# Performance work log

Measured on AMD Instinct MI355X. Metric: run time of the kernel, lower is better.

Reference implementation:

```python
import jax, jax.numpy as jnp
import numpy as np

B, L, D, W = 4, 256, 256, 8  # batch, seq_len, d_model, context_window
NS_EPS = 1e-7


def setup_inputs() -> dict:
    key = jax.random.key(0)
    ks = jax.random.split(key, 12)
    f = lambda k, s: jax.random.normal(k, s, dtype=jnp.float32)
    sD = 1.0 / np.sqrt(D)
    return {
        "x": f(ks[0], (B, L, D)),
        "k_aligned": jnp.tanh(f(ks[1], (B, L, D))),  # QKProjectionLayer applies tanh upstream
        "v": f(ks[2], (B, L, D)),
        "M_prev": f(ks[3], (B, D, D)) * 0.01,
        "S_prev": jnp.zeros((B, D, D), jnp.float32),
        # polynomial feature coeffs: phi(k) = c1*k + c2*k^2 (degree 2, dim-preserving)
        "poly_coeffs": jnp.stack([jnp.ones((D,), jnp.float32), 0.1 * jnp.ones((D,), jnp.float32)])
        + 0.01 * f(ks[4], (2, D)),
        "alpha_W": f(ks[5], (D, D)) * sD, "alpha_b": jnp.zeros((D,), jnp.float32),
        "eta_W": f(ks[6], (D, D)) * sD, "eta_b": jnp.zeros((D,), jnp.float32),
        "theta_W": f(ks[7], (D, D)) * sD, "theta_b": jnp.zeros((D,), jnp.float32),
        "gamma_W": f(ks[8], (D,)) * sD, "gamma_b": jnp.zeros((1,), jnp.float32),
        "out_W": f(ks[9], (D, D)) * sD, "out_b": jnp.zeros((D,), jnp.float32),
    }


def _newton_schulz_1(S):
    # NS_K with K=1: X <- 1.5*X - 0.5*X X^T X after Frobenius normalization
    norm = jnp.sqrt(jnp.sum(S * S, axis=(-2, -1), keepdims=True)) + NS_EPS
    X = S / norm
    return 1.5 * X - 0.5 * jnp.einsum('bij,bkj,bkl->bil', X, X, X)


def reference(x, k_aligned, v, M_prev, S_prev, poly_coeffs,
              alpha_W, alpha_b, eta_W, eta_b, theta_W, theta_b,
              gamma_W, gamma_b, out_W, out_b):
    Bn, Ln, Dn = x.shape
    # polynomial feature layer (dim-preserving, degree 2)
    k_phi = poly_coeffs[0] * k_aligned + poly_coeffs[1] * k_aligned ** 2  # [B,L,D]
    # per-token gates (precomputed, pure linear+sigmoid)
    alpha = jax.nn.sigmoid(x @ alpha_W.T + alpha_b)          # [B,L,D]
    eta = jax.nn.sigmoid(x @ eta_W.T + eta_b) * 0.1          # [B,L,D]
    theta = jax.nn.sigmoid(x @ theta_W.T + theta_b)          # [B,L,D]
    gamma = jax.nn.sigmoid(jnp.einsum('bld,d->bl', x, gamma_W) + gamma_b[0])  # [B,L]
    c_arr = jnp.minimum(jnp.arange(Ln) + 1, W).astype(x.dtype)  # actual window length per step

    to_t = lambda a: jnp.moveaxis(a, 1, 0)  # [B,L,...] -> [L,B,...]
    xs = (to_t(k_phi), to_t(v), to_t(gamma), to_t(alpha), to_t(eta), to_t(theta), c_arr)

    buf_k = jnp.zeros((Bn, W, Dn), x.dtype)  # sliding window of phi(k); zero pads contribute 0
    buf_v = jnp.zeros((Bn, W, Dn), x.dtype)
    buf_g = jnp.zeros((Bn, W), x.dtype)

    def step(carry, xt):
        M, S, bk, bv, bg = carry
        k_t, v_t, g_t, a_t, e_t, th_t, c_t = xt
        bk = jnp.concatenate([bk[:, 1:], k_t[:, None]], axis=1)
        bv = jnp.concatenate([bv[:, 1:], v_t[:, None]], axis=1)
        bg = jnp.concatenate([bg[:, 1:], g_t[:, None]], axis=1)
        # Omega gradient: sum_i gamma_i * (M phi(k_i) - v_i) outer phi(k_i) / c
        pred = jnp.einsum('bde,bwe->bwd', M, bk)
        err = pred - bv
        grad = jnp.einsum('bw,bwd,bwe->bde', bg, err, bk) / c_t
        S = th_t[..., None] * S + grad
        S_ortho = _newton_schulz_1(S)
        M = a_t[..., None] * M - e_t[..., None] * S_ortho
        y = jnp.einsum('bde,be->bd', M, k_t)
        return (M, S, bk, bv, bg), y

    (M, S, _, _, _), ys = jax.lax.scan(step, (M_prev, S_prev, buf_k, buf_v, buf_g), xs)
    output = jnp.moveaxis(ys, 0, 1) @ out_W.T + out_b  # out_proj per token
    return (output, M, S)
```

## Files before the change

kernel.cpp:

```cpp
#include <hip/hip_runtime.h>

#define Bn 4
#define Ln 256
#define Dn 256
#define Wn 8
#define BLD (Bn*Ln*Dn)
#define BDD (Bn*Dn*Dn)

typedef float  floatx4 __attribute__((ext_vector_type(4)));
typedef short  short8  __attribute__((ext_vector_type(8)));

__device__ __forceinline__ unsigned f2bf(float x) {
    unsigned u = __float_as_uint(x);
    return (u + 0x7FFFu + ((u >> 16) & 1u)) >> 16;
}
__device__ __forceinline__ unsigned long long packbf4(floatx4 v) {
    unsigned lo = f2bf(v[0]) | (f2bf(v[1]) << 16);
    unsigned hi = f2bf(v[2]) | (f2bf(v[3]) << 16);
    return (unsigned long long)lo | ((unsigned long long)hi << 32);
}
union BF8 { short8 s8; unsigned long long u[2]; };

__global__ __launch_bounds__(256) void kphi_gamma_kernel(
    const float* __restrict__ k_al, const float* __restrict__ x,
    const float* __restrict__ poly, const float* __restrict__ gW,
    const float* __restrict__ gb, float* __restrict__ kphi,
    float* __restrict__ gamma)
{
    int wg = blockIdx.x, tid = threadIdx.x;
    int wave = tid >> 6, lane = tid & 63;
    int n = wg * 4 + wave;
    float gacc = 0.f;
#pragma unroll
    for (int c = 0; c < 4; ++c) {
        int e = lane + 64 * c;
        float kv = k_al[n * Dn + e];
        kphi[n * Dn + e] = poly[e] * kv + poly[Dn + e] * kv * kv;
        gacc += x[n * Dn + e] * gW[e];
    }
#pragma unroll
    for (int off = 32; off; off >>= 1) gacc += __shfl_xor(gacc, off);
    if (lane == 0) gamma[n] = 1.f / (1.f + expf(-(gacc + gb[0])));
}

template <int ACT>
__global__ __launch_bounds__(256) void gemm_act_kernel(
    const float* __restrict__ In, const float* __restrict__ Wm,
    const float* __restrict__ bias, float* __restrict__ Out)
{
    __shared__ float ldsX[32 * 64];
    __shared__ float ldsW[64 * 65];
    int n0 = blockIdx.x * 32;
    int m0 = blockIdx.y * 64;
    int tid = threadIdx.x;
    float acc[8] = {0, 0, 0, 0, 0, 0, 0, 0};
    for (int j0 = 0; j0 < 256; j0 += 64) {
#pragma unroll
        for (int q = 0; q < 2; ++q) {
            int fi = tid + 256 * q; int row = fi >> 4; int c4 = (fi & 15) << 2;
            *(float4*)&ldsX[row * 64 + c4] =
                *(const float4*)&In[(n0 + row) * 256 + j0 + c4];
        }
#pragma unroll
        for (int q = 0; q < 4; ++q) {
            int fi = tid + 256 * q; int row = fi >> 4; int c4 = (fi & 15) << 2;
            float4 vv = *(const float4*)&Wm[(m0 + row) * 256 + j0 + c4];
            ldsW[(c4 + 0) * 65 + row] = vv.x;
            ldsW[(c4 + 1) * 65 + row] = vv.y;
            ldsW[(c4 + 2) * 65 + row] = vv.z;
            ldsW[(c4 + 3) * 65 + row] = vv.w;
        }
        __syncthreads();
        int m = tid & 63, ng = tid >> 6;
        for (int j = 0; j < 64; ++j) {
            float wv = ldsW[j * 65 + m];
#pragma unroll
            for (int r = 0; r < 8; ++r) acc[r] += ldsX[(ng * 8 + r) * 64 + j] * wv;
        }
        __syncthreads();
    }
    int m = tid & 63, ng = tid >> 6;
    float bv = bias[m0 + m];
#pragma unroll
    for (int r = 0; r < 8; ++r) {
        float vv = acc[r] + bv;
        if (ACT == 1) vv = 1.f / (1.f + expf(-vv));
        if (ACT == 2) vv = 0.1f / (1.f + expf(-vv));
        Out[(n0 + ng * 8 + r) * 256 + m0 + m] = vv;
    }
}

__global__ __launch_bounds__(64) void kgram_kernel(
    const float* __restrict__ kphi, float* __restrict__ Kall)
{
    int t = blockIdx.x, b = blockIdx.y, tid = threadIdx.x;
    int wa = tid >> 3, wb = tid & 7;
    int ta = t - 7 + wa, tb = t - 7 + wb;
    float g = 0.f;
    if (ta >= 0 && tb >= 0) {
        const float* pa = &kphi[(b * Ln + ta) * Dn];
        const float* pb = &kphi[(b * Ln + tb) * Dn];
        for (int j = 0; j < Dn; j += 4) {
            floatx4 x1 = *(const floatx4*)&pa[j];
            floatx4 x2 = *(const floatx4*)&pb[j];
            g += x1[0]*x2[0] + x1[1]*x2[1] + x1[2]*x2[2] + x1[3]*x2[3];
        }
    }
    Kall[(b * Ln + t) * 64 + tid] = g;
}

__global__ __launch_bounds__(256) void prologue_kernel(
    const float* __restrict__ Mprev, const float* __restrict__ Sprev,
    float* __restrict__ M, float* __restrict__ S,
    float* __restrict__ ys, float* __restrict__ errp)
{
    int gidx = blockIdx.x * 256 + threadIdx.x;
    ((float4*)M)[gidx] = ((const float4*)Mprev)[gidx];
    ((float4*)S)[gidx] = ((const float4*)Sprev)[gidx];
    float4 z = {0.f, 0.f, 0.f, 0.f};
    ((float4*)ys)[gidx] = z;
    if (gidx < 16384) ((float4*)errp)[gidx] = z;
}

__global__ __launch_bounds__(256) void tinit_kernel(
    const float* __restrict__ Sprev, float* __restrict__ Tg0)
{
    const int wg = blockIdx.x, tid = threadIdx.x;
    const int b = wg >> 4, rem = wg & 15;
    const int i0 = (rem >> 2) * 64, l0 = (rem & 3) * 64;
    const int wid = tid >> 6, lane = tid & 63;
    const int lme = lane & 15, hi = lane >> 4;
    floatx4 acc[4];
#pragma unroll
    for (int lt = 0; lt < 4; ++lt) acc[lt] = (floatx4){0.f,0.f,0.f,0.f};
#pragma unroll
    for (int kc = 0; kc < 8; ++kc) {
        int kb2 = kc*32 + hi*8;
        floatx4 a0 = *(const floatx4*)&Sprev[(size_t)(b*256 + i0 + wid*16 + lme)*256 + kb2];
        floatx4 a1 = *(const floatx4*)&Sprev[(size_t)(b*256 + i0 + wid*16 + lme)*256 + kb2 + 4];
        BF8 ua; ua.u[0] = packbf4(a0); ua.u[1] = packbf4(a1);
#pragma unroll
        for (int lt = 0; lt < 4; ++lt) {
            int brow = l0 + lt*16 + lme;
            floatx4 b0 = *(const floatx4*)&Sprev[(size_t)(b*256 + brow)*256 + kb2];
            floatx4 b1 = *(const floatx4*)&Sprev[(size_t)(b*256 + brow)*256 + kb2 + 4];
            BF8 ub; ub.u[0] = packbf4(b0); ub.u[1] = packbf4(b1);
            acc[lt] = __builtin_amdgcn_mfma_f32_16x16x32_bf16(ua.s8, ub.s8, acc[lt], 0,0,0);
        }
    }
#pragma unroll
    for (int lt = 0; lt < 4; ++lt)
#pragma unroll
        for (int g = 0; g < 4; ++g)
            Tg0[(size_t)(b*256 + i0 + wid*16 + (hi<<2) + g)*256 + l0 + lt*16 + lme]
                = acc[lt][g];
}

__global__ __launch_bounds__(256) void err0_kernel(
    const float* __restrict__ kphi, const float* __restrict__ Mprev,
    float* __restrict__ errp)
{
    __shared__ float kW2[Wn * 256];
    const int wg = blockIdx.x, tid = threadIdx.x;
    const int b = wg >> 4, rem = wg & 15;
    const int s = rem & 3;
    const int i0 = (rem >> 2) * 64, l0 = (rem & 3) * 64;
    const int wid = tid >> 6, lane = tid & 63;
    const int lme = lane & 15, hi = lane >> 4;
    const int ibr = i0 + wid * 16 + (hi << 2);
#pragma unroll
    for (int q = 0; q < 2; ++q) {
        int w = q*4 + (tid >> 6);
        int c4 = (tid & 63) << 2;
        floatx4 kv = {0.f,0.f,0.f,0.f};
        if (w == 7) kv = *(const floatx4*)&kphi[(size_t)(b*Ln)*Dn + c4];
        *(floatx4*)&kW2[w*256 + c4] = kv;
    }
    __syncthreads();
    float M_reg[16];
#pragma unroll
    for (int lt = 0; lt < 4; ++lt)
#pragma unroll
        for (int g = 0; g < 4; ++g)
            M_reg[lt*4+g] = Mprev[(size_t)(b*256 + ibr + g)*256 + l0 + lt*16 + lme];
#pragma unroll
    for (int w = 0; w < 8; ++w) {
        float pd[4] = {0.f,0.f,0.f,0.f};
#pragma unroll
        for (int lt = 0; lt < 4; ++lt) {
            float kv2 = kW2[w*256 + l0 + lt*16 + lme];
#pragma unroll
            for (int g = 0; g < 4; ++g) pd[g] += M_reg[lt*4+g] * kv2;
        }
#pragma unroll
        for (int g = 0; g < 4; ++g) {
            pd[g] += __shfl_xor(pd[g], 1); pd[g] += __shfl_xor(pd[g], 2);
            pd[g] += __shfl_xor(pd[g], 4); pd[g] += __shfl_xor(pd[g], 8);
        }
        if (lme == 0)
#pragma unroll
            for (int g = 0; g < 4; ++g)
                errp[(size_t)((s*2 + 0)*4 + b)*2048 + w*256 + ibr + g] = pd[g];
    }
}

__global__ __launch_bounds__(256) void phaseA_kernel(
    const float* __restrict__ kphi, const float* __restrict__ vin,
    const float* __restrict__ gammaB, const float* __restrict__ thetaB,
    float* __restrict__ Sg, unsigned short* __restrict__ STg,
    float* __restrict__ u_buf, float* __restrict__ a_buf,
    const float* __restrict__ errp, float* __restrict__ normp, int t)
{
    __shared__ float usl[Wn * 16];
    __shared__ float kWA[Wn * 260];
    __shared__ float Sl[16 * 260];
    __shared__ float wsum[4];
    const int wg = blockIdx.x, tid = threadIdx.x;
    const int b = wg >> 4, rem = wg & 15;
    const int d0 = rem << 4;
    const int wid = tid >> 6, lane = tid & 63;
    const int r = tid >> 4, m = tid & 15;
    const int e0 = m * 16;
    const int cwin = (t + 1 < Wn) ? (t + 1) : Wn;
    const float invc = 1.f / (float)cwin;
    const int p = t & 1;

    if (tid < 128) {
        int w_a = tid >> 4, rr_a = tid & 15;
        float ep = 0.f;
#pragma unroll
        for (int sl = 0; sl < 4; ++sl)
            ep += errp[(size_t)((sl*2 + p)*4 + b)*2048 + w_a*256 + d0 + rr_a];
        int tok = t - 7 + w_a;
        float uu = 0.f;
        if (tok >= 0)
            uu = gammaB[b*Ln + tok] * invc *
                 (ep - vin[(size_t)(b*Ln + tok)*Dn + d0 + rr_a]);
        usl[w_a*16 + rr_a] = uu;
        u_buf[(size_t)(b*8 + w_a)*256 + d0 + rr_a] = uu;
    } else {
        int idx = tid - 128;
        int w = idx >> 4, seg = idx & 15;
        int tk = t - 7 + w;
#pragma unroll
        for (int q = 0; q < 4; ++q) {
            floatx4 kv = {0.f,0.f,0.f,0.f};
            if (tk >= 0)
                kv = *(const floatx4*)&kphi[(size_t)(b*Ln + tk)*Dn + seg*16 + q*4];
            *(floatx4*)&kWA[w*260 + seg*16 + q*4] = kv;
        }
    }
    __syncthreads();

    floatx4 S_reg[4];
#pragma unroll
    for (int cq = 0; cq < 4; ++cq)
        S_reg[cq] = *(const floatx4*)&Sg[(size_t)(b*256 + d0 + r)*256 + e0 + cq*4];
    {
        float qw[8] = {0,0,0,0,0,0,0,0};
#pragma unroll
        for (int cq = 0; cq < 4; ++cq) {
            floatx4 sv = S_reg[cq];
#pragma unroll
            for (int w = 0; w < 8; ++w) {
                floatx4 kv = *(const floatx4*)&kWA[w*260 + e0 + cq*4];
                qw[w] += sv[0]*kv[0] + sv[1]*kv[1] + sv[2]*kv[2] + sv[3]*kv[3];
            }
        }
#pragma unroll
        for (int w = 0; w < 8; ++w) {
            qw[w] += __shfl_xor(qw[w], 1); qw[w] += __shfl_xor(qw[w], 2);
            qw[w] += __shfl_xor(qw[w], 4); qw[w] += __shfl_xor(qw[w], 8);
        }
        if (m < 8) {
            float th = thetaB[(size_t)(b*Ln + t)*Dn + d0 + r];
            a_buf[(size_t)(b*8 + m)*256 + d0 + r] = th * qw[m];
        }
    }
    {
        float th = thetaB[(size_t)(b*Ln + t)*Dn + d0 + r];
        float uu[8];
#pragma unroll
        for (int w = 0; w < 8; ++w) uu[w] = usl[w*16 + r];
        float sumsq = 0.f;
#pragma unroll
        for (int cq = 0; cq < 4; ++cq) {
            floatx4 sv = th * S_reg[cq];
#pragma unroll
            for (int w = 0; w < 8; ++w) {
                floatx4 kv = *(const floatx4*)&kWA[w*260 + e0 + cq*4];
                sv += uu[w] * kv;
            }
            S_reg[cq] = sv;
            sumsq += sv[0]*sv[0] + sv[1]*sv[1] + sv[2]*sv[2] + sv[3]*sv[3];
        }
#pragma unroll
        for (int off = 32; off; off >>= 1) sumsq += __shfl_xor(sumsq, off);
        if (lane == 0) wsum[wid] = sumsq;
    }
    {
#pragma unroll
        for (int cq = 0; cq < 4; ++cq) {
            *(floatx4*)&Sg[(size_t)(b*256 + d0 + r)*256 + e0 + cq*4] = S_reg[cq];
            *(floatx4*)&Sl[r*260 + e0 + cq*4] = S_reg[cq];
        }
        __syncthreads();
        int l = tid;
        unsigned dw[8];
#pragma unroll
        for (int j = 0; j < 8; ++j)
            dw[j] = f2bf(Sl[(2*j)*260 + l]) | (f2bf(Sl[(2*j+1)*260 + l]) << 16);
        float4 p0 = { __uint_as_float(dw[0]), __uint_as_float(dw[1]),
                      __uint_as_float(dw[2]), __uint_as_float(dw[3]) };
        float4 p1 = { __uint_as_float(dw[4]), __uint_as_float(dw[5]),
                      __uint_as_float(dw[6]), __uint_as_float(dw[7]) };
        char* dstp = (char*)STg + ((size_t)(b*256 + l)*256 + d0)*2;
        *(float4*)dstp = p0;
        *(float4*)(dstp + 16) = p1;
        if (tid == 0)
            normp[b*16 + rem] = wsum[0] + wsum[1] + wsum[2] + wsum[3];
    }
}

__global__ __launch_bounds__(256) void phaseC_kernel(
    const float* __restrict__ kphi, const float* __restrict__ alphaB,
    const float* __restrict__ etaB, const float* __restrict__ thetaB,
    const float* __restrict__ Kall,
    const unsigned short* __restrict__ STg,
    const float* __restrict__ u_buf, const float* __restrict__ a_buf,
    const float* __restrict__ normp,
    const float* __restrict__ Tin, float* __restrict__ Tout,
    float* __restrict__ Mg, float* __restrict__ ys,
    float* __restrict__ errp, int t)
{
    __shared__ float smem[8448 + 2048*3 + 256 + 256 + 64 + 16 + 2048];
    char*  STb  = (char*)smem;
    float* uvp  = smem + 8448;
    float* avp  = smem + 10496;
    float* cvp  = smem + 12544;
    float* thv  = smem + 14592;
    float* kT   = smem + 14848;
    float* Kl   = smem + 15104;
    float* nrml = smem + 15168;
    float* kW2  = smem + 15184;

    const int wg = blockIdx.x, tid = threadIdx.x;
    const int b = wg >> 4, rem = wg & 15;
    const int s = rem & 3;
    const int i0 = (rem >> 2) * 64, l0 = (rem & 3) * 64;
    const int wid = tid >> 6, lane = tid & 63;
    const int lme = lane & 15, hi = lane >> 4;
    const int ibr = i0 + wid * 16 + (hi << 2);

    {
        int lq = tid >> 2, kq = (tid & 3) * 64;
        const char* src = (const char*)STg + ((size_t)(b*256 + l0 + lq)*256 + kq)*2;
        size_t rb0 = (size_t)lq*528 + (size_t)kq*2;
        unsigned swz = (unsigned)((lq & 8) << 1);
#pragma unroll
        for (int q = 0; q < 8; ++q) {
            float4 vv = *(const float4*)(src + q*16);
            *(float4*)(STb + ((rb0 + q*16) ^ swz)) = vv;
        }
        *(floatx4*)&uvp[tid*8]     = *(const floatx4*)&u_buf[(size_t)b*2048 + tid*8];
        *(floatx4*)&uvp[tid*8 + 4] = *(const floatx4*)&u_buf[(size_t)b*2048 + tid*8 + 4];
        *(floatx4*)&avp[tid*8]     = *(const floatx4*)&a_buf[(size_t)b*2048 + tid*8];
        *(floatx4*)&avp[tid*8 + 4] = *(const floatx4*)&a_buf[(size_t)b*2048 + tid*8 + 4];
        if (tid < 16) nrml[tid] = normp[b*16 + tid];
        if (tid < 64) {
            *(floatx4*)&thv[tid*4] = *(const floatx4*)&thetaB[(size_t)(b*Ln + t)*Dn + tid*4];
            *(floatx4*)&kT[tid*4]  = *(const floatx4*)&kphi[(size_t)(b*Ln + t)*Dn + tid*4];
        }
        if (tid < 16)
            *(floatx4*)&Kl[tid*4] = *(const floatx4*)&Kall[(size_t)(b*Ln + t)*64 + tid*4];
        if (t < Ln - 1) {
#pragma unroll
            for (int q = 0; q < 2; ++q) {
                int w = q*4 + (tid >> 6);
                int c4 = (tid & 63) << 2;
                int tk = t + 1 - 7 + w;
                floatx4 kv = {0.f,0.f,0.f,0.f};
                if (tk >= 0) kv = *(const floatx4*)&kphi[(size_t)(b*Ln + tk)*Dn + c4];
                *(floatx4*)&kW2[w*256 + c4] = kv;
            }
        }
    }
    __syncthreads();

#pragma unroll
    for (int q = 0; q < 8; ++q) {
        int idx = q*256 + tid;
        int w = idx >> 8, e = idx & 255;
        float sv = avp[idx];
#pragma unroll
        for (int w2 = 0; w2 < 8; ++w2)
            sv += 0.5f * Kl[w*8 + w2] * uvp[w2*256 + e];
        cvp[idx] = sv;
    }
    __syncthreads();

    floatx4 T_reg[16];
    {
        const float* Trow = &Tin[(size_t)(b*256 + i0 + wid*16 + lme)*256];
        int i = i0 + wid*16 + lme;
        float thi = thv[i];
        float ui8[8], ci8[8];
#pragma unroll
        for (int w = 0; w < 8; ++w) { ui8[w] = uvp[w*256 + i]; ci8[w] = cvp[w*256 + i]; }
#pragma unroll
        for (int kc = 0; kc < 8; ++kc) {
            int k0 = kc*32 + hi*8;
            floatx4 t0 = *(const floatx4*)&Trow[k0];
            floatx4 t1 = *(const floatx4*)&Trow[k0 + 4];
            floatx4 th0 = *(const floatx4*)&thv[k0];
            floatx4 th1 = *(const floatx4*)&thv[k0 + 4];
            t0 = (thi * th0) * t0;
            t1 = (thi * th1) * t1;
#pragma unroll
            for (int w = 0; w < 8; ++w) {
                floatx4 uk0 = *(const floatx4*)&uvp[w*256 + k0];
                floatx4 uk1 = *(const floatx4*)&uvp[w*256 + k0 + 4];
                floatx4 ck0 = *(const floatx4*)&cvp[w*256 + k0];
                floatx4 ck1 = *(const floatx4*)&cvp[w*256 + k0 + 4];
                t0 += ui8[w]*ck0 + ci8[w]*uk0;
                t1 += ui8[w]*ck1 + ci8[w]*uk1;
            }
            T_reg[kc*2+0] = t0;
            T_reg[kc*2+1] = t1;
        }
        if (s == 0) {
            float* Torow = &Tout[(size_t)(b*256 + i0 + wid*16 + lme)*256];
#pragma unroll
            for (int kc = 0; kc < 8; ++kc) {
                *(floatx4*)&Torow[kc*32 + hi*8]     = T_reg[kc*2+0];
                *(floatx4*)&Torow[kc*32 + hi*8 + 4] = T_reg[kc*2+1];
            }
        }
    }

    floatx4 acc[4];
#pragma unroll
    for (int lt = 0; lt < 4; ++lt) acc[lt] = (floatx4){0.f,0.f,0.f,0.f};
#pragma unroll
    for (int kc = 0; kc < 8; ++kc) {
        BF8 ua; ua.u[0] = packbf4(T_reg[kc*2]); ua.u[1] = packbf4(T_reg[kc*2+1]);
        int kbyte = kc*64 + hi*16;
#pragma unroll
        for (int lt = 0; lt < 4; ++lt) {
            int row = lt*16 + lme;
            short8 bf = *(const short8*)(STb +
                (((size_t)row*528 + kbyte) ^ (unsigned)((row & 8) << 1)));
            acc[lt] = __builtin_amdgcn_mfma_f32_16x16x32_bf16(ua.s8, bf, acc[lt], 0,0,0);
        }
    }

    {
        float nsq = 0.f;
#pragma unroll
        for (int q = 0; q < 16; ++q) nsq += nrml[q];
        float nrm = sqrtf(nsq) + 1e-7f;
        float inv_n = 1.f / nrm;
        float w1 = 1.5f * inv_n;
        float w3 = 0.5f * inv_n * inv_n * inv_n;
        float alv[4], etv[4], kvr[4], M_reg[16];
#pragma unroll
        for (int g = 0; g < 4; ++g) {
            alv[g] = alphaB[(size_t)(b*Ln + t)*Dn + ibr + g];
            etv[g] = etaB[(size_t)(b*Ln + t)*Dn + ibr + g];
        }
#pragma unroll
        for (int lt = 0; lt < 4; ++lt) kvr[lt] = kT[l0 + lt*16 + lme];
#pragma unroll
        for (int lt = 0; lt < 4; ++lt)
#pragma unroll
            for (int g = 0; g < 4; ++g)
                M_reg[lt*4+g] = Mg[(size_t)(b*256 + ibr + g)*256 + l0 + lt*16 + lme];
        float py[4] = {0.f,0.f,0.f,0.f};
#pragma unroll
        for (int lt = 0; lt < 4; ++lt)
#pragma unroll
            for (int g = 0; g < 4; ++g) {
                int l_loc = lt*16 + lme;
                unsigned short sb = *(const unsigned short*)(STb +
                    (((size_t)l_loc*528 + (size_t)(ibr + g)*2) ^ (unsigned)((l_loc & 8) << 1)));
                float s_il = __uint_as_float(((unsigned)sb) << 16);
                float ns = w1 * s_il - w3 * acc[lt][g];
                float mn = alv[g] * M_reg[lt*4+g] - etv[g] * ns;
                M_reg[lt*4+g] = mn;
                py[g] += mn * kvr[lt];
                Mg[(size_t)(b*256 + ibr + g)*256 + l0 + l_loc] = mn;
            }
#pragma unroll
        for (int g = 0; g < 4; ++g) {
            py[g] += __shfl_xor(py[g], 1); py[g] += __shfl_xor(py[g], 2);
            py[g] += __shfl_xor(py[g], 4); py[g] += __shfl_xor(py[g], 8);
            if (lme == 0) atomicAdd(&ys[(size_t)(b*Ln + t)*Dn + ibr + g], py[g]);
        }

        if (t < Ln - 1) {
            const int p2 = (t + 1) & 1;
#pragma unroll
            for (int w = 0; w < 8; ++w) {
                float pd[4] = {0.f,0.f,0.f,0.f};
#pragma unroll
                for (int lt = 0; lt < 4; ++lt) {
                    float kv2 = kW2[w*256 + l0 + lt*16 + lme];
#pragma unroll
                    for (int g = 0; g < 4; ++g) pd[g] += M_reg[lt*4+g] * kv2;
                }
#pragma unroll
                for (int g = 0; g < 4; ++g) {
                    pd[g] += __shfl_xor(pd[g], 1); pd[g] += __shfl_xor(pd[g], 2);
                    pd[g] += __shfl_xor(pd[g], 4); pd[g] += __shfl_xor(pd[g], 8);
                }
                if (lme == 0)
#pragma unroll
                    for (int g = 0; g < 4; ++g)
                        errp[(size_t)((s*2 + p2)*4 + b)*2048 + w*256 + ibr + g] = pd[g];
            }
        }
    }
}

extern "C" void kernel_launch(void* const* d_in, const int* in_sizes, int n_in,
                              void* d_out, int out_size, void* d_ws, size_t ws_size,
                              hipStream_t stream)
{
    const float* x       = (const float*)d_in[0];
    const float* k_al    = (const float*)d_in[1];
    const float* v       = (const float*)d_in[2];
    const float* M_prev  = (const float*)d_in[3];
    const float* S_prev  = (const float*)d_in[4];
    const float* poly    = (const float*)d_in[5];
    const float* alpha_W = (const float*)d_in[6];
    const float* alpha_b = (const float*)d_in[7];
    const float* eta_W   = (const float*)d_in[8];
    const float* eta_b   = (const float*)d_in[9];
    const float* theta_W = (const float*)d_in[10];
    const float* theta_b = (const float*)d_in[11];
    const float* gamma_W = (const float*)d_in[12];
    const float* gamma_b = (const float*)d_in[13];
    const float* out_W   = (const float*)d_in[14];
    const float* out_b   = (const float*)d_in[15];

    float* ws = (float*)d_ws;
    float* kphi    = ws;
    float* alphaB  = kphi   + BLD;
    float* etaB    = alphaB + BLD;
    float* thetaB  = etaB   + BLD;
    float* gammaB  = thetaB + BLD;
    float* Kall    = gammaB + Bn*Ln;
    float* STg_f   = Kall   + Bn*Ln*64;
    float* u_bufp  = STg_f  + 131072;
    float* a_bufp  = u_bufp + Bn*Wn*Dn;
    float* errp    = a_bufp + Bn*Wn*Dn;
    float* normp   = errp   + 65536;
    float* ysb     = normp  + 64;
    float* Tg0     = ysb    + BLD;
    float* Tg1     = Tg0    + BDD;

    float* out_y = (float*)d_out;
    float* outM  = out_y + BLD;
    float* outS  = outM + BDD;

    hipLaunchKernelGGL(kphi_gamma_kernel, dim3(256), dim3(256), 0, stream,
                       k_al, x, poly, gamma_W, gamma_b, kphi, gammaB);
    hipLaunchKernelGGL((gemm_act_kernel<1>), dim3(32, 4), dim3(256), 0, stream,
                       x, alpha_W, alpha_b, alphaB);
    hipLaunchKernelGGL((gemm_act_kernel<2>), dim3(32, 4), dim3(256), 0, stream,
                       x, eta_W, eta_b, etaB);
    hipLaunchKernelGGL((gemm_act_kernel<1>), dim3(32, 4), dim3(256), 0, stream,
                       x, theta_W, theta_b, thetaB);
    hipLaunchKernelGGL(kgram_kernel, dim3(Ln, Bn), dim3(64), 0, stream,
                       kphi, Kall);
    hipLaunchKernelGGL(prologue_kernel, dim3(256), dim3(256), 0, stream,
                       M_prev, S_prev, outM, outS, ysb, errp);
    hipLaunchKernelGGL(tinit_kernel, dim3(64), dim3(256), 0, stream,
                       S_prev, Tg0);
    hipLaunchKernelGGL(err0_kernel, dim3(64), dim3(256), 0, stream,
                       kphi, M_prev, errp);

    for (int t = 0; t < Ln; ++t) {
        float* Tin  = (t & 1) ? Tg1 : Tg0;
        float* Tout = (t & 1) ? Tg0 : Tg1;
        hipLaunchKernelGGL(phaseA_kernel, dim3(64), dim3(256), 0, stream,
                           kphi, v, gammaB, thetaB, outS,
                           (unsigned short*)STg_f, u_bufp, a_bufp,
                           errp, normp, t);
        hipLaunchKernelGGL(phaseC_kernel, dim3(64), dim3(256), 0, stream,
                           kphi, alphaB, etaB, thetaB, Kall,
                           (const unsigned short*)STg_f, u_bufp, a_bufp, normp,
                           Tin, Tout, outM, ysb, errp, t);
    }

    hipLaunchKernelGGL((gemm_act_kernel<0>), dim3(32, 4), dim3(256), 0, stream,
                       ysb, out_W, out_b, out_y);
}
```

Before: 5.326 ms.

## Fuse per-step phaseA and phaseC into one step kernel with analytic Frobenius norm

```diff
diff --git a/kernel.cpp b/kernel.cpp
--- a/kernel.cpp
+++ b/kernel.cpp
@@ -111,12 +111,12 @@
 
 __global__ __launch_bounds__(256) void prologue_kernel(
     const float* __restrict__ Mprev, const float* __restrict__ Sprev,
-    float* __restrict__ M, float* __restrict__ S,
+    float* __restrict__ M, float* __restrict__ S0,
     float* __restrict__ ys, float* __restrict__ errp)
 {
     int gidx = blockIdx.x * 256 + threadIdx.x;
     ((float4*)M)[gidx] = ((const float4*)Mprev)[gidx];
-    ((float4*)S)[gidx] = ((const float4*)Sprev)[gidx];
+    ((float4*)S0)[gidx] = ((const float4*)Sprev)[gidx];
     float4 z = {0.f, 0.f, 0.f, 0.f};
     ((float4*)ys)[gidx] = z;
     if (gidx < 16384) ((float4*)errp)[gidx] = z;
@@ -158,7 +158,8 @@
 
 __global__ __launch_bounds__(256) void err0_kernel(
     const float* __restrict__ kphi, const float* __restrict__ Mprev,
-    float* __restrict__ errp)
+    const float* __restrict__ Sprev, float* __restrict__ errp,
+    float* __restrict__ rowsq0)
 {
     __shared__ float kW2[Wn * 256];
     const int wg = blockIdx.x, tid = threadIdx.x;
@@ -202,200 +203,184 @@
             for (int g = 0; g < 4; ++g)
                 errp[(size_t)((s*2 + 0)*4 + b)*2048 + w*256 + ibr + g] = pd[g];
     }
-}
-
-__global__ __launch_bounds__(256) void phaseA_kernel(
+    if (rem == 0) {
+        const float* Srow = &Sprev[(size_t)(b*256 + tid)*256];
+        float sq = 0.f;
+        for (int j = 0; j < 256; j += 4) {
+            floatx4 sv = *(const floatx4*)&Srow[j];
+            sq += sv[0]*sv[0] + sv[1]*sv[1] + sv[2]*sv[2] + sv[3]*sv[3];
+        }
+        rowsq0[b*256 + tid] = sq;
+    }
+}
+
+#define OFF_STB   0
+#define OFF_UV    8448
+#define OFF_QV    10496
+#define OFF_CV    12544
+#define OFF_TH    14592
+#define OFF_KWA   14848
+#define OFF_KW2   16928
+#define OFF_KL    18976
+#define OFF_RED   19040
+#define SMEM_FL   19056
+
+__global__ __launch_bounds__(256) void step_kernel(
     const float* __restrict__ kphi, const float* __restrict__ vin,
-    const float* __restrict__ gammaB, const float* __restrict__ thetaB,
-    float* __restrict__ Sg, unsigned short* __restrict__ STg,
-    float* __restrict__ u_buf, float* __restrict__ a_buf,
-    const float* __restrict__ errp, float* __restrict__ normp, int t)
-{
-    __shared__ float usl[Wn * 16];
-    __shared__ float kWA[Wn * 260];
-    __shared__ float Sl[16 * 260];
-    __shared__ float wsum[4];
+    const float* __restrict__ gammaB, const float* __restrict__ alphaB,
+    const float* __restrict__ etaB, const float* __restrict__ thetaB,
+    const float* __restrict__ Kall,
+    const float* __restrict__ S_in, float* __restrict__ S_out,
+    const float* __restrict__ Tin, float* __restrict__ Tout,
+    const float* __restrict__ rowsq_in, float* __restrict__ rowsq_out,
+    float* __restrict__ errp, float* __restrict__ Mg, float* __restrict__ ys,
+    int t)
+{
+    __shared__ float smem[SMEM_FL];
+    char*  STb = (char*)(smem + OFF_STB);
+    float* uv  = smem + OFF_UV;
+    float* qv  = smem + OFF_QV;
+    float* cv  = smem + OFF_CV;
+    float* thv = smem + OFF_TH;
+    float* kWA = smem + OFF_KWA;
+    float* kW2 = smem + OFF_KW2;
+    float* Kl  = smem + OFF_KL;
+    float* red = smem + OFF_RED;
+
     const int wg = blockIdx.x, tid = threadIdx.x;
     const int b = wg >> 4, rem = wg & 15;
+    const int s = rem & 3;
+    const int i0 = (rem >> 2) * 64, l0 = (rem & 3) * 64;
     const int d0 = rem << 4;
     const int wid = tid >> 6, lane = tid & 63;
+    const int lme = lane & 15, hi = lane >> 4;
+    const int ibr = i0 + wid * 16 + (hi << 2);
     const int r = tid >> 4, m = tid & 15;
     const int e0 = m * 16;
     const int cwin = (t + 1 < Wn) ? (t + 1) : Wn;
     const float invc = 1.f / (float)cwin;
     const int p = t & 1;
 
-    if (tid < 128) {
-        int w_a = tid >> 4, rr_a = tid & 15;
-        float ep = 0.f;
-#pragma unroll
-        for (int sl = 0; sl < 4; ++sl)
-            ep += errp[(size_t)((sl*2 + p)*4 + b)*2048 + w_a*256 + d0 + rr_a];
-        int tok = t - 7 + w_a;
-        float uu = 0.f;
-        if (tok >= 0)
-            uu = gammaB[b*Ln + tok] * invc *
-                 (ep - vin[(size_t)(b*Ln + tok)*Dn + d0 + rr_a]);
-        usl[w_a*16 + rr_a] = uu;
-        u_buf[(size_t)(b*8 + w_a)*256 + d0 + rr_a] = uu;
-    } else {
-        int idx = tid - 128;
-        int w = idx >> 4, seg = idx & 15;
+#pragma unroll
+    for (int qq = 0; qq < 2; ++qq) {
+        int idx = qq*256 + tid;
+        int w = idx >> 6, c4 = (idx & 63) * 4;
         int tk = t - 7 + w;
-#pragma unroll
-        for (int q = 0; q < 4; ++q) {
-            floatx4 kv = {0.f,0.f,0.f,0.f};
-            if (tk >= 0)
-                kv = *(const floatx4*)&kphi[(size_t)(b*Ln + tk)*Dn + seg*16 + q*4];
-            *(floatx4*)&kWA[w*260 + seg*16 + q*4] = kv;
+        floatx4 kv = {0,0,0,0};
+        if (tk >= 0) kv = *(const floatx4*)&kphi[(size_t)(b*Ln + tk)*Dn + c4];
+        *(floatx4*)&kWA[w*260 + c4] = kv;
+        floatx4 kv2 = {0,0,0,0};
+        int tk2 = t + 1 - 7 + w;
+        if (t + 1 < Ln && tk2 >= 0)
+            kv2 = *(const floatx4*)&kphi[(size_t)(b*Ln + tk2)*Dn + c4];
+        *(floatx4*)&kW2[w*256 + c4] = kv2;
+    }
+    if (tid < 64)
+        *(floatx4*)&thv[tid*4] = *(const floatx4*)&thetaB[(size_t)(b*Ln + t)*Dn + tid*4];
+    if (tid < 16)
+        *(floatx4*)&Kl[tid*4] = *(const floatx4*)&Kall[(size_t)(b*Ln + t)*64 + tid*4];
+    {
+#pragma unroll
+        for (int w = 0; w < 8; ++w) {
+            float ep = 0.f;
+#pragma unroll
+            for (int sl = 0; sl < 4; ++sl)
+                ep += errp[(size_t)((sl*2 + p)*4 + b)*2048 + w*256 + tid];
+            int tok = t - 7 + w;
+            float uu = 0.f;
+            if (tok >= 0)
+                uu = gammaB[b*Ln + tok] * invc *
+                     (ep - vin[(size_t)(b*Ln + tok)*Dn + tid]);
+            uv[w*256 + tid] = uu;
         }
     }
     __syncthreads();
 
-    floatx4 S_reg[4];
-#pragma unroll
-    for (int cq = 0; cq < 4; ++cq)
-        S_reg[cq] = *(const floatx4*)&Sg[(size_t)(b*256 + d0 + r)*256 + e0 + cq*4];
-    {
+    {
+        const float* Srow = &S_in[(size_t)(b*256 + tid)*256];
         float qw[8] = {0,0,0,0,0,0,0,0};
+        for (int j = 0; j < 256; j += 4) {
+            floatx4 sv = *(const floatx4*)&Srow[j];
+#pragma unroll
+            for (int w = 0; w < 8; ++w) {
+                floatx4 kv = *(const floatx4*)&kWA[w*260 + j];
+                qw[w] += sv[0]*kv[0] + sv[1]*kv[1] + sv[2]*kv[2] + sv[3]*kv[3];
+            }
+        }
+#pragma unroll
+        for (int w = 0; w < 8; ++w) qv[w*256 + tid] = qw[w];
+    }
+
+    {
+        float th_r = thetaB[(size_t)(b*Ln + t)*Dn + d0 + r];
+        float uu8[8];
+#pragma unroll
+        for (int w = 0; w < 8; ++w) uu8[w] = uv[w*256 + d0 + r];
 #pragma unroll
         for (int cq = 0; cq < 4; ++cq) {
-            floatx4 sv = S_reg[cq];
+            floatx4 sv = *(const floatx4*)&S_in[(size_t)(b*256 + d0 + r)*256 + e0 + cq*4];
+            sv = th_r * sv;
 #pragma unroll
             for (int w = 0; w < 8; ++w) {
                 floatx4 kv = *(const floatx4*)&kWA[w*260 + e0 + cq*4];
-                qw[w] += sv[0]*kv[0] + sv[1]*kv[1] + sv[2]*kv[2] + sv[3]*kv[3];
-            }
-        }
+                sv += uu8[w] * kv;
+            }
+            *(floatx4*)&S_out[(size_t)(b*256 + d0 + r)*256 + e0 + cq*4] = sv;
+        }
+    }
+
+    float uL[8];
+#pragma unroll
+    for (int w = 0; w < 8; ++w) uL[w] = uv[w*256 + tid];
+    {
+        float th_d = thv[tid];
+        for (int j0 = 0; j0 < 64; j0 += 4) {
+            floatx4 sv = *(const floatx4*)&S_in[(size_t)(b*256 + tid)*256 + l0 + j0];
+            sv = th_d * sv;
+#pragma unroll
+            for (int w = 0; w < 8; ++w) {
+                floatx4 kv = *(const floatx4*)&kWA[w*260 + l0 + j0];
+                sv += uL[w] * kv;
+            }
+#pragma unroll
+            for (int jj = 0; jj < 4; ++jj) {
+                int row = j0 + jj;
+                *(unsigned short*)(STb +
+                    (((size_t)row*528 + 2*(size_t)tid) ^ (unsigned)((row & 8) << 1))) =
+                    (unsigned short)f2bf(sv[jj]);
+            }
+        }
+    }
+
+    {
+        float th_d = thv[tid];
+        float cross = 0.f, quad = 0.f;
 #pragma unroll
         for (int w = 0; w < 8; ++w) {
-            qw[w] += __shfl_xor(qw[w], 1); qw[w] += __shfl_xor(qw[w], 2);
-            qw[w] += __shfl_xor(qw[w], 4); qw[w] += __shfl_xor(qw[w], 8);
-        }
-        if (m < 8) {
-            float th = thetaB[(size_t)(b*Ln + t)*Dn + d0 + r];
-            a_buf[(size_t)(b*8 + m)*256 + d0 + r] = th * qw[m];
-        }
-    }
-    {
-        float th = thetaB[(size_t)(b*Ln + t)*Dn + d0 + r];
-        float uu[8];
-#pragma unroll
-        for (int w = 0; w < 8; ++w) uu[w] = usl[w*16 + r];
-        float sumsq = 0.f;
-#pragma unroll
-        for (int cq = 0; cq < 4; ++cq) {
-            floatx4 sv = th * S_reg[cq];
-#pragma unroll
-            for (int w = 0; w < 8; ++w) {
-                floatx4 kv = *(const floatx4*)&kWA[w*260 + e0 + cq*4];
-                sv += uu[w] * kv;
-            }
-            S_reg[cq] = sv;
-            sumsq += sv[0]*sv[0] + sv[1]*sv[1] + sv[2]*sv[2] + sv[3]*sv[3];
-        }
-#pragma unroll
-        for (int off = 32; off; off >>= 1) sumsq += __shfl_xor(sumsq, off);
-        if (lane == 0) wsum[wid] = sumsq;
-    }
-    {
-#pragma unroll
-        for (int cq = 0; cq < 4; ++cq) {
-            *(floatx4*)&Sg[(size_t)(b*256 + d0 + r)*256 + e0 + cq*4] = S_reg[cq];
-            *(floatx4*)&Sl[r*260 + e0 + cq*4] = S_reg[cq];
-        }
-        __syncthreads();
-        int l = tid;
-        unsigned dw[8];
-#pragma unroll
-        for (int j = 0; j < 8; ++j)
-            dw[j] = f2bf(Sl[(2*j)*260 + l]) | (f2bf(Sl[(2*j+1)*260 + l]) << 16);
-        float4 p0 = { __uint_as_float(dw[0]), __uint_as_float(dw[1]),
-                      __uint_as_float(dw[2]), __uint_as_float(dw[3]) };
-        float4 p1 = { __uint_as_float(dw[4]), __uint_as_float(dw[5]),
-                      __uint_as_float(dw[6]), __uint_as_float(dw[7]) };
-        char* dstp = (char*)STg + ((size_t)(b*256 + l)*256 + d0)*2;
-        *(float4*)dstp = p0;
-        *(float4*)(dstp + 16) = p1;
-        if (tid == 0)
-            normp[b*16 + rem] = wsum[0] + wsum[1] + wsum[2] + wsum[3];
-    }
-}
-
-__global__ __launch_bounds__(256) void phaseC_kernel(
-    const float* __restrict__ kphi, const float* __restrict__ alphaB,
-    const float* __restrict__ etaB, const float* __restrict__ thetaB,
-    const float* __restrict__ Kall,
-    const unsigned short* __restrict__ STg,
-    const float* __restrict__ u_buf, const float* __restrict__ a_buf,
-    const float* __restrict__ normp,
-    const float* __restrict__ Tin, float* __restrict__ Tout,
-    float* __restrict__ Mg, float* __restrict__ ys,
-    float* __restrict__ errp, int t)
-{
-    __shared__ float smem[8448 + 2048*3 + 256 + 256 + 64 + 16 + 2048];
-    char*  STb  = (char*)smem;
-    float* uvp  = smem + 8448;
-    float* avp  = smem + 10496;
-    float* cvp  = smem + 12544;
-    float* thv  = smem + 14592;
-    float* kT   = smem + 14848;
-    float* Kl   = smem + 15104;
-    float* nrml = smem + 15168;
-    float* kW2  = smem + 15184;
-
-    const int wg = blockIdx.x, tid = threadIdx.x;
-    const int b = wg >> 4, rem = wg & 15;
-    const int s = rem & 3;
-    const int i0 = (rem >> 2) * 64, l0 = (rem & 3) * 64;
-    const int wid = tid >> 6, lane = tid & 63;
-    const int lme = lane & 15, hi = lane >> 4;
-    const int ibr = i0 + wid * 16 + (hi << 2);
-
-    {
-        int lq = tid >> 2, kq = (tid & 3) * 64;
-        const char* src = (const char*)STg + ((size_t)(b*256 + l0 + lq)*256 + kq)*2;
-        size_t rb0 = (size_t)lq*528 + (size_t)kq*2;
-        unsigned swz = (unsigned)((lq & 8) << 1);
-#pragma unroll
-        for (int q = 0; q < 8; ++q) {
-            float4 vv = *(const float4*)(src + q*16);
-            *(float4*)(STb + ((rb0 + q*16) ^ swz)) = vv;
-        }
-        *(floatx4*)&uvp[tid*8]     = *(const floatx4*)&u_buf[(size_t)b*2048 + tid*8];
-        *(floatx4*)&uvp[tid*8 + 4] = *(const floatx4*)&u_buf[(size_t)b*2048 + tid*8 + 4];
-        *(floatx4*)&avp[tid*8]     = *(const floatx4*)&a_buf[(size_t)b*2048 + tid*8];
-        *(floatx4*)&avp[tid*8 + 4] = *(const floatx4*)&a_buf[(size_t)b*2048 + tid*8 + 4];
-        if (tid < 16) nrml[tid] = normp[b*16 + tid];
-        if (tid < 64) {
-            *(floatx4*)&thv[tid*4] = *(const floatx4*)&thetaB[(size_t)(b*Ln + t)*Dn + tid*4];
-            *(floatx4*)&kT[tid*4]  = *(const floatx4*)&kphi[(size_t)(b*Ln + t)*Dn + tid*4];
-        }
-        if (tid < 16)
-            *(floatx4*)&Kl[tid*4] = *(const floatx4*)&Kall[(size_t)(b*Ln + t)*64 + tid*4];
-        if (t < Ln - 1) {
-#pragma unroll
-            for (int q = 0; q < 2; ++q) {
-                int w = q*4 + (tid >> 6);
-                int c4 = (tid & 63) << 2;
-                int tk = t + 1 - 7 + w;
-                floatx4 kv = {0.f,0.f,0.f,0.f};
-                if (tk >= 0) kv = *(const floatx4*)&kphi[(size_t)(b*Ln + tk)*Dn + c4];
-                *(floatx4*)&kW2[w*256 + c4] = kv;
-            }
-        }
+            cross += uL[w] * qv[w*256 + tid];
+            float kk = 0.f;
+#pragma unroll
+            for (int w2 = 0; w2 < 8; ++w2) kk += Kl[w*8 + w2] * uL[w2];
+            quad += uL[w] * kk;
+        }
+        float rq = th_d*th_d*rowsq_in[b*256 + tid] + 2.f*th_d*cross + quad;
+        if (rem == 0) rowsq_out[b*256 + tid] = rq;
+        float sum = rq;
+#pragma unroll
+        for (int off = 32; off; off >>= 1) sum += __shfl_xor(sum, off);
+        if (lane == 0) red[wid] = sum;
     }
     __syncthreads();
 
 #pragma unroll
-    for (int q = 0; q < 8; ++q) {
-        int idx = q*256 + tid;
+    for (int qq = 0; qq < 8; ++qq) {
+        int idx = qq*256 + tid;
         int w = idx >> 8, e = idx & 255;
-        float sv = avp[idx];
+        float sv = thv[e] * qv[w*256 + e];
 #pragma unroll
         for (int w2 = 0; w2 < 8; ++w2)
-            sv += 0.5f * Kl[w*8 + w2] * uvp[w2*256 + e];
-        cvp[idx] = sv;
+            sv += 0.5f * Kl[w*8 + w2] * uv[w2*256 + e];
+        cv[w*256 + e] = sv;
     }
     __syncthreads();
 
@@ -406,7 +391,7 @@
         float thi = thv[i];
         float ui8[8], ci8[8];
 #pragma unroll
-        for (int w = 0; w < 8; ++w) { ui8[w] = uvp[w*256 + i]; ci8[w] = cvp[w*256 + i]; }
+        for (int w = 0; w < 8; ++w) { ui8[w] = uv[w*256 + i]; ci8[w] = cv[w*256 + i]; }
 #pragma unroll
         for (int kc = 0; kc < 8; ++kc) {
             int k0 = kc*32 + hi*8;
@@ -418,10 +403,10 @@
             t1 = (thi * th1) * t1;
 #pragma unroll
             for (int w = 0; w < 8; ++w) {
-                floatx4 uk0 = *(const floatx4*)&uvp[w*256 + k0];
-                floatx4 uk1 = *(const floatx4*)&uvp[w*256 + k0 + 4];
-                floatx4 ck0 = *(const floatx4*)&cvp[w*256 + k0];
-                floatx4 ck1 = *(const floatx4*)&cvp[w*256 + k0 + 4];
+                floatx4 uk0 = *(const floatx4*)&uv[w*256 + k0];
+                floatx4 uk1 = *(const floatx4*)&uv[w*256 + k0 + 4];
+                floatx4 ck0 = *(const floatx4*)&cv[w*256 + k0];
+                floatx4 ck1 = *(const floatx4*)&cv[w*256 + k0 + 4];
                 t0 += ui8[w]*ck0 + ci8[w]*uk0;
                 t1 += ui8[w]*ck1 + ci8[w]*uk1;
             }
@@ -457,7 +442,7 @@
     {
         float nsq = 0.f;
 #pragma unroll
-        for (int q = 0; q < 16; ++q) nsq += nrml[q];
+        for (int q = 0; q < 16; ++q) nsq += red[q];
         float nrm = sqrtf(nsq) + 1e-7f;
         float inv_n = 1.f / nrm;
         float w1 = 1.5f * inv_n;
@@ -469,7 +454,7 @@
             etv[g] = etaB[(size_t)(b*Ln + t)*Dn + ibr + g];
         }
 #pragma unroll
-        for (int lt = 0; lt < 4; ++lt) kvr[lt] = kT[l0 + lt*16 + lme];
+        for (int lt = 0; lt < 4; ++lt) kvr[lt] = kWA[7*260 + l0 + lt*16 + lme];
 #pragma unroll
         for (int lt = 0; lt < 4; ++lt)
 #pragma unroll
@@ -496,7 +481,6 @@
             py[g] += __shfl_xor(py[g], 4); py[g] += __shfl_xor(py[g], 8);
             if (lme == 0) atomicAdd(&ys[(size_t)(b*Ln + t)*Dn + ibr + g], py[g]);
         }
-
         if (t < Ln - 1) {
             const int p2 = (t + 1) & 1;
 #pragma unroll
@@ -550,12 +534,11 @@
     float* thetaB  = etaB   + BLD;
     float* gammaB  = thetaB + BLD;
     float* Kall    = gammaB + Bn*Ln;
-    float* STg_f   = Kall   + Bn*Ln*64;
-    float* u_bufp  = STg_f  + 131072;
-    float* a_bufp  = u_bufp + Bn*Wn*Dn;
-    float* errp    = a_bufp + Bn*Wn*Dn;
-    float* normp   = errp   + 65536;
-    float* ysb     = normp  + 64;
+    float* S1      = Kall   + Bn*Ln*64;
+    float* errp    = S1     + BDD;
+    float* rowsq0b = errp   + 65536;
+    float* rowsq1b = rowsq0b + 1024;
+    float* ysb     = rowsq1b + 1024;
     float* Tg0     = ysb    + BLD;
     float* Tg1     = Tg0    + BDD;
 
@@ -578,19 +561,19 @@
     hipLaunchKernelGGL(tinit_kernel, dim3(64), dim3(256), 0, stream,
                        S_prev, Tg0);
     hipLaunchKernelGGL(err0_kernel, dim3(64), dim3(256), 0, stream,
-                       kphi, M_prev, errp);
+                       kphi, M_prev, S_prev, errp, rowsq0b);
 
     for (int t = 0; t < Ln; ++t) {
-        float* Tin  = (t & 1) ? Tg1 : Tg0;
-        float* Tout = (t & 1) ? Tg0 : Tg1;
-        hipLaunchKernelGGL(phaseA_kernel, dim3(64), dim3(256), 0, stream,
-                           kphi, v, gammaB, thetaB, outS,
-                           (unsigned short*)STg_f, u_bufp, a_bufp,
-                           errp, normp, t);
-        hipLaunchKernelGGL(phaseC_kernel, dim3(64), dim3(256), 0, stream,
-                           kphi, alphaB, etaB, thetaB, Kall,
-                           (const unsigned short*)STg_f, u_bufp, a_bufp, normp,
-                           Tin, Tout, outM, ysb, errp, t);
+        float* S_in   = (t & 1) ? S1 : outS;
+        float* S_out  = (t & 1) ? outS : S1;
+        float* Tin    = (t & 1) ? Tg1 : Tg0;
+        float* Tout   = (t & 1) ? Tg0 : Tg1;
+        float* rq_in  = (t & 1) ? rowsq1b : rowsq0b;
+        float* rq_out = (t & 1) ? rowsq0b : rowsq1b;
+        hipLaunchKernelGGL(step_kernel, dim3(64), dim3(256), 0, stream,
+                           kphi, v, gammaB, alphaB, etaB, thetaB, Kall,
+                           S_in, S_out, Tin, Tout, rq_in, rq_out,
+                           errp, outM, ysb, t);
     }
 
     hipLaunchKernelGGL((gemm_act_kernel<0>), dim3(32, 4), dim3(256), 0, stream,
```

Result: slower. 7.731 ms (+45.1%).
